# Optimization experiments

Measured on AMD Instinct MI355X. Metric: run time of the kernel, lower is better.

## Reference

```python
import jax, jax.numpy as jnp
import numpy as np

V, E, D = 50000, 800000, 128
EH, NH = 128, 128  # edge_hidden, node_hidden


def setup_inputs() -> dict:
    key = jax.random.key(0)
    ks = jax.random.split(key, 12)
    h = jax.random.normal(ks[0], (V, D), dtype=jnp.float32)
    edge_index = jax.random.randint(ks[1], (2, E), 0, V, dtype=jnp.int64)
    s = 0.02
    # edge MLP: Linear(2D->EH), Linear(EH->EH), Linear(EH->NH)
    W1 = jax.random.normal(ks[2], (2 * D, EH), dtype=jnp.float32) * s
    b1 = jnp.zeros((EH,), dtype=jnp.float32)
    W2 = jax.random.normal(ks[3], (EH, EH), dtype=jnp.float32) * s
    b2 = jnp.zeros((EH,), dtype=jnp.float32)
    W3 = jax.random.normal(ks[4], (EH, NH), dtype=jnp.float32) * s
    b3 = jnp.zeros((NH,), dtype=jnp.float32)
    # node MLP: Linear(D+NH->NH), Linear(NH->NH)
    Wn1 = jax.random.normal(ks[5], (D + NH, NH), dtype=jnp.float32) * s
    bn1 = jnp.zeros((NH,), dtype=jnp.float32)
    Wn2 = jax.random.normal(ks[6], (NH, NH), dtype=jnp.float32) * s
    bn2 = jnp.zeros((NH,), dtype=jnp.float32)
    return {"h": h, "edge_index": edge_index, "W1": W1, "b1": b1, "W2": W2,
            "b2": b2, "W3": W3, "b3": b3, "Wn1": Wn1, "bn1": bn1,
            "Wn2": Wn2, "bn2": bn2}


def reference(h, edge_index, W1, b1, W2, b2, W3, b3, Wn1, bn1, Wn2, bn2):
    src, dst = edge_index[0], edge_index[1]
    # gather node pairs -> edge features (E, 2D)
    edge_feat = jnp.concatenate([h[src], h[dst]], axis=-1)
    # 3-layer edge MLP
    m = jax.nn.relu(edge_feat @ W1 + b1)
    m = jax.nn.relu(m @ W2 + b2)
    messages = m @ W3 + b3                       # (E, NH)
    # scatter-add into destination nodes
    agg = jax.ops.segment_sum(messages, dst, num_segments=h.shape[0])  # (V, NH)
    # node MLP on [h, agg]
    x = jnp.concatenate([h, agg], axis=-1)       # (V, D+NH)
    out = jax.nn.relu(x @ Wn1 + bn1) @ Wn2 + bn2  # (V, NH)
    return out
```

## Files before the change

kernel.cpp:

```cpp
#include <hip/hip_runtime.h>

#define NV 50000
#define NE 800000
#define CVT_N 1600000
#define TR_N  81920
#define W3N_N 16384
#define B3N_N 128
#define NB1 49

typedef _Float16 f16x8 __attribute__((ext_vector_type(8)));
typedef _Float16 f16x4 __attribute__((ext_vector_type(4)));
typedef float    f32x4 __attribute__((ext_vector_type(4)));

static __device__ __forceinline__ f32x4 mfma16(f16x8 a, f16x8 b, f32x4 c) {
  return __builtin_amdgcn_mfma_f32_16x16x32_f16(a, b, c, 0, 0, 0);
}

__global__ void prep_kernel(const float* __restrict__ h, _Float16* __restrict__ hf,
    const float* __restrict__ W1, const float* __restrict__ W2, const float* __restrict__ W3,
    const float* __restrict__ Wn1, const float* __restrict__ Wn2, const float* __restrict__ b3,
    _Float16* __restrict__ w1st, _Float16* __restrict__ w1dt, _Float16* __restrict__ w2t,
    _Float16* __restrict__ wn1c, _Float16* __restrict__ wn2t, float* __restrict__ b3n,
    const int* __restrict__ ei, int* __restrict__ counts)
{
  int i = blockIdx.x * blockDim.x + threadIdx.x;
  if (i < CVT_N) {
    f32x4 v = reinterpret_cast<const f32x4*>(h)[i];
    f16x4 o;
    o[0] = (_Float16)v[0]; o[1] = (_Float16)v[1]; o[2] = (_Float16)v[2]; o[3] = (_Float16)v[3];
    reinterpret_cast<f16x4*>(hf)[i] = o;
    return;
  }
  i -= CVT_N;
  if (i < TR_N) {
    int seg = i >> 14;
    int j = i & 16383;
    int f = j >> 7, k = j & 127;
    switch (seg) {
      case 0: w1st[j] = (_Float16)W1[k * 128 + f]; break;
      case 1: w1dt[j] = (_Float16)W1[(k + 128) * 128 + f]; break;
      case 2: w2t[j]  = (_Float16)W2[k * 128 + f]; break;
      case 3: wn1c[f * 256 + k] = (_Float16)Wn1[k * 128 + f]; break;
      case 4: wn2t[j] = (_Float16)Wn2[k * 128 + f]; break;
    }
    return;
  }
  i -= TR_N;
  if (i < W3N_N) {
    int f = i >> 7, ii = i & 127;
    float a = 0.f;
    for (int j = 0; j < 128; j++) a += W3[ii * 128 + j] * Wn1[(128 + j) * 128 + f];
    wn1c[f * 256 + 128 + ii] = (_Float16)a;
    return;
  }
  i -= W3N_N;
  if (i < B3N_N) {
    float a = 0.f;
    for (int j = 0; j < 128; j++) a += b3[j] * Wn1[(128 + j) * 128 + i];
    b3n[i] = a;
    return;
  }
  i -= B3N_N;
  if (i < NE) atomicAdd(&counts[ei[NE + i]], 1);
}

__global__ __launch_bounds__(1024)
void bsum_kernel(const int* __restrict__ counts, int* __restrict__ bsum) {
  __shared__ int red[1024];
  const int t = threadIdx.x;
  int i = blockIdx.x * 1024 + t;
  red[t] = (i < NV) ? counts[i] : 0;
  __syncthreads();
  for (int off = 512; off > 0; off >>= 1) {
    if (t < off) red[t] += red[t + off];
    __syncthreads();
  }
  if (t == 0) bsum[blockIdx.x] = red[0];
}

__global__ void bscan_kernel(const int* __restrict__ bsum, int* __restrict__ boff) {
  if (threadIdx.x == 0 && blockIdx.x == 0) {
    int run = 0;
    for (int b = 0; b < NB1; b++) { boff[b] = run; run += bsum[b]; }
    boff[NB1] = run;
  }
}

__global__ __launch_bounds__(1024)
void offs_kernel(const int* __restrict__ counts, const int* __restrict__ boff,
                 int* __restrict__ offsets, int* __restrict__ cursor) {
  __shared__ int s[1024];
  const int t = threadIdx.x;
  int i = blockIdx.x * 1024 + t;
  int v = (i < NV) ? counts[i] : 0;
  s[t] = v;
  __syncthreads();
  for (int off = 1; off < 1024; off <<= 1) {
    int x = (t >= off) ? s[t - off] : 0;
    __syncthreads();
    s[t] += x;
    __syncthreads();
  }
  if (i < NV) {
    int excl = boff[blockIdx.x] + s[t] - v;
    offsets[i] = excl;
    cursor[i] = excl;
    if (i == NV - 1) offsets[NV] = boff[blockIdx.x] + s[t];
  }
}

__global__ void permute_kernel(const int* __restrict__ ei, int* __restrict__ cursor,
                               int2* __restrict__ pairs) {
  int e = blockIdx.x * blockDim.x + threadIdx.x;
  if (e < NE) {
    int s = ei[e], d = ei[NE + e];
    int pos = atomicAdd(&cursor[d], 1);
    pairs[pos] = make_int2(s, d);
  }
}

static __device__ __forceinline__ void gemm128_rows(
    const _Float16* __restrict__ hf, const int* nid, const _Float16* __restrict__ At,
    const float* __restrict__ bias, _Float16* __restrict__ Out,
    int nbase, int l15, int quad)
{
  f32x4 acc[8][4];
#pragma unroll
  for (int mt = 0; mt < 8; mt++)
#pragma unroll
    for (int nt = 0; nt < 4; nt++)
      acc[mt][nt] = (f32x4){0.f, 0.f, 0.f, 0.f};

  f16x8 Bc[4], Bn[4];
#pragma unroll
  for (int nt = 0; nt < 4; nt++)
    Bc[nt] = *reinterpret_cast<const f16x8*>(hf + (long long)nid[nt] * 128 + quad * 8);
#pragma unroll
  for (int s = 0; s < 4; s++) {
    if (s < 3) {
#pragma unroll
      for (int nt = 0; nt < 4; nt++)
        Bn[nt] = *reinterpret_cast<const f16x8*>(hf + (long long)nid[nt] * 128 + (s + 1) * 32 + quad * 8);
    }
    const int k = s * 32 + quad * 8;
#pragma unroll
    for (int mt = 0; mt < 8; mt++) {
      f16x8 A = *reinterpret_cast<const f16x8*>(At + (mt * 16 + l15) * 128 + k);
#pragma unroll
      for (int nt = 0; nt < 4; nt++)
        acc[mt][nt] = mfma16(A, Bc[nt], acc[mt][nt]);
    }
#pragma unroll
    for (int nt = 0; nt < 4; nt++) Bc[nt] = Bn[nt];
  }
#pragma unroll
  for (int mt = 0; mt < 8; mt++) {
    f32x4 bb = bias ? *reinterpret_cast<const f32x4*>(bias + mt * 16 + quad * 4)
                    : (f32x4){0.f, 0.f, 0.f, 0.f};
#pragma unroll
    for (int nt = 0; nt < 4; nt++) {
      int n = nbase + nt * 16 + l15;
      if (n < NV) {
        f16x4 o;
#pragma unroll
        for (int r = 0; r < 4; r++) o[r] = (_Float16)(acc[mt][nt][r] + bb[r]);
        *reinterpret_cast<f16x4*>(Out + (long long)n * 128 + mt * 16 + quad * 4) = o;
      }
    }
  }
}

__global__ __launch_bounds__(256, 2)
void h1_kernel(const _Float16* __restrict__ hf, const float* __restrict__ b1,
               const _Float16* __restrict__ w1st, const _Float16* __restrict__ w1dt,
               _Float16* __restrict__ H1s, _Float16* __restrict__ H1d)
{
  const int t = threadIdx.x;
  const int lane = t & 63, wave = t >> 6;
  const int quad = lane >> 4, l15 = lane & 15;
  const int nbase = blockIdx.x * 256 + wave * 64;
  int nid[4];
#pragma unroll
  for (int nt = 0; nt < 4; nt++) {
    int n = nbase + nt * 16 + l15;
    nid[nt] = n < NV ? n : NV - 1;
  }
  if (blockIdx.y == 0) gemm128_rows(hf, nid, w1st, nullptr, H1s, nbase, l15, quad);
  else                 gemm128_rows(hf, nid, w1dt, b1,      H1d, nbase, l15, quad);
}

__global__ __launch_bounds__(128, 2)
void edge_kernel(const _Float16* __restrict__ H1s, const _Float16* __restrict__ H1d,
                 const int2* __restrict__ pairs,
                 const _Float16* __restrict__ w2t, const float* __restrict__ b2,
                 float* __restrict__ agg2)
{
  __shared__ __align__(16) _Float16 M2t[128 * 128];
  __shared__ int sdst[128];
  __shared__ int segdst[128];
  __shared__ __align__(8) unsigned char sseg8[128];
  __shared__ unsigned long long wmask[2];
  __shared__ int snbr[2];

  const int t = threadIdx.x;
  const int lane = t & 63, wave = t >> 6;
  const int quad = lane >> 4, l15 = lane & 15;
  const int ebase = blockIdx.x * 128;
  const int wbase = wave * 64;

  { int2 pr = pairs[ebase + t]; sdst[t] = pr.y; }
  if (t == 0) snbr[0] = (ebase > 0) ? pairs[ebase - 1].y : -1;
  if (t == 1) snbr[1] = (ebase + 128 < NE) ? pairs[ebase + 128].y : -1;

  int esrc[4], edst[4];
#pragma unroll
  for (int et = 0; et < 4; et++) {
    int2 pr = pairs[ebase + wbase + et * 16 + l15];
    esrc[et] = pr.x; edst[et] = pr.y;
  }

  f16x8 m1f[4][4];
#pragma unroll
  for (int et = 0; et < 4; et++) {
#pragma unroll
    for (int s = 0; s < 4; s++) {
      f16x8 a = *reinterpret_cast<const f16x8*>(H1s + (long long)esrc[et] * 128 + s * 32 + quad * 8);
      f16x8 b = *reinterpret_cast<const f16x8*>(H1d + (long long)edst[et] * 128 + s * 32 + quad * 8);
      f16x8 o = a + b;
#pragma unroll
      for (int j = 0; j < 8; j++) o[j] = o[j] > (_Float16)0 ? o[j] : (_Float16)0;
      m1f[et][s] = o;
    }
  }

  __syncthreads();
  {
    bool flag = (t > 0) && (sdst[t] != sdst[t - 1]);
    unsigned long long bm = __ballot(flag);
    if (lane == 0) wmask[wave] = bm;
    int pre = __popcll(bm & ((1ull << lane) - 1ull)) + (flag ? 1 : 0);
    __syncthreads();
    int sid = pre + (wave ? (int)__popcll(wmask[0]) : 0);
    sseg8[t] = (unsigned char)sid;
    if (flag || t == 0) segdst[sid] = sdst[t];
  }

  float b2v[8];
#pragma unroll
  for (int ft = 0; ft < 8; ft++) b2v[ft] = b2[ft * 16 + l15];

  f32x4 acc[4][8];
#pragma unroll
  for (int et = 0; et < 4; et++)
#pragma unroll
    for (int ft = 0; ft < 8; ft++)
      acc[et][ft] = (f32x4){0.f, 0.f, 0.f, 0.f};

#pragma unroll
  for (int s = 0; s < 4; s++) {
    const int k = s * 32 + quad * 8;
#pragma unroll
    for (int ft = 0; ft < 8; ft++) {
      f16x8 B = *reinterpret_cast<const f16x8*>(w2t + (ft * 16 + l15) * 128 + k);
#pragma unroll
      for (int et = 0; et < 4; et++)
        acc[et][ft] = mfma16(m1f[et][s], B, acc[et][ft]);
    }
  }
#pragma unroll
  for (int et = 0; et < 4; et++) {
    const int g = wave * 16 + et * 4 + quad;
#pragma unroll
    for (int ft = 0; ft < 8; ft++) {
      const int f = ft * 16 + l15;
      f16x4 o;
#pragma unroll
      for (int r = 0; r < 4; r++) {
        float x = acc[et][ft][r] + b2v[ft];
        o[r] = (_Float16)(x > 0.f ? x : 0.f);
      }
      *reinterpret_cast<f16x4*>(&M2t[f * 128 + ((g ^ (l15 << 1)) * 4)]) = o;
    }
  }
  __syncthreads();

  const int nseg = (int)__popcll(wmask[0]) + (int)__popcll(wmask[1]) + 1;
  const int nmt = (nseg + 15) >> 4;
  const bool openL = (sdst[0] == snbr[0]);
  const bool openR = (sdst[127] == snbr[1]);

  f16x8 Bf[4][4];
#pragma unroll
  for (int fl = 0; fl < 4; fl++) {
    const int f = (wave * 4 + fl) * 16 + l15;
#pragma unroll
    for (int s = 0; s < 4; s++) {
      const int g0 = s * 8 + quad * 2;
      Bf[fl][s] = *reinterpret_cast<const f16x8*>(&M2t[f * 128 + ((g0 ^ (l15 << 1)) * 4)]);
    }
  }
  unsigned long long segb[4];
#pragma unroll
  for (int s = 0; s < 4; s++)
    segb[s] = *reinterpret_cast<const unsigned long long*>(&sseg8[s * 32 + quad * 8]);

  for (int mt = 0; mt < nmt; mt++) {
    const int myseg = mt * 16 + l15;
    f32x4 racc[4];
#pragma unroll
    for (int fl = 0; fl < 4; fl++) racc[fl] = (f32x4){0.f, 0.f, 0.f, 0.f};
#pragma unroll
    for (int s = 0; s < 4; s++) {
      f16x8 S;
#pragma unroll
      for (int j = 0; j < 8; j++)
        S[j] = ((int)((segb[s] >> (8 * j)) & 255ull) == myseg) ? (_Float16)1 : (_Float16)0;
#pragma unroll
      for (int fl = 0; fl < 4; fl++)
        racc[fl] = mfma16(S, Bf[fl][s], racc[fl]);
    }
#pragma unroll
    for (int fl = 0; fl < 4; fl++) {
      const int f = (wave * 4 + fl) * 16 + l15;
#pragma unroll
      for (int r = 0; r < 4; r++) {
        const int sg = mt * 16 + quad * 4 + r;
        if (sg < nseg) {
          float v = racc[fl][r];
          float* p = agg2 + (long long)segdst[sg] * 128 + f;
          const bool at = (sg == 0 && openL) || (sg == nseg - 1 && openR);
          if (at) unsafeAtomicAdd(p, v); else *p = v;
        }
      }
    }
  }
}

__global__ __launch_bounds__(256, 2)
void node_kernel(const _Float16* __restrict__ hf, const float* __restrict__ agg2,
                 const int* __restrict__ offsets,
                 const _Float16* __restrict__ wn1c, const float* __restrict__ bn1,
                 const float* __restrict__ b3n,
                 const _Float16* __restrict__ wn2t, const float* __restrict__ bn2,
                 float* __restrict__ out)
{
  __shared__ __align__(16) _Float16 M[256 * 128];
  const int t = threadIdx.x;
  const int lane = t & 63, wave = t >> 6;
  const int quad = lane >> 4, l15 = lane & 15;
  const int wbase = wave * 64;
  const int nbase = blockIdx.x * 256 + wbase;

  int nid[4]; float fcnt[4];
#pragma unroll
  for (int nt = 0; nt < 4; nt++) {
    int n = nbase + nt * 16 + l15;
    nid[nt] = n < NV ? n : NV - 1;
    fcnt[nt] = (n < NV) ? (float)(offsets[n + 1] - offsets[n]) : 0.f;
  }

  f32x4 acc[8][4];
#pragma unroll
  for (int mt = 0; mt < 8; mt++)
#pragma unroll
    for (int nt = 0; nt < 4; nt++)
      acc[mt][nt] = (f32x4){0.f, 0.f, 0.f, 0.f};

  f16x8 Bc[4], Bn[4];
#pragma unroll
  for (int nt = 0; nt < 4; nt++)
    Bc[nt] = *reinterpret_cast<const f16x8*>(hf + (long long)nid[nt] * 128 + quad * 8);
#pragma unroll
  for (int s = 0; s < 8; s++) {
    if (s < 7) {
      const int sn = s + 1;
      if (sn < 4) {
#pragma unroll
        for (int nt = 0; nt < 4; nt++)
          Bn[nt] = *reinterpret_cast<const f16x8*>(hf + (long long)nid[nt] * 128 + sn * 32 + quad * 8);
      } else {
#pragma unroll
        for (int nt = 0; nt < 4; nt++) {
          const float* ap = agg2 + (long long)nid[nt] * 128 + (sn - 4) * 32 + quad * 8;
          f32x4 a0 = *reinterpret_cast<const f32x4*>(ap);
          f32x4 a1 = *reinterpret_cast<const f32x4*>(ap + 4);
          f16x8 bb;
#pragma unroll
          for (int j = 0; j < 4; j++) { bb[j] = (_Float16)a0[j]; bb[4 + j] = (_Float16)a1[j]; }
          Bn[nt] = bb;
        }
      }
    }
    const int k = s * 32 + quad * 8;
#pragma unroll
    for (int mt = 0; mt < 8; mt++) {
      f16x8 A = *reinterpret_cast<const f16x8*>(wn1c + (mt * 16 + l15) * 256 + k);
#pragma unroll
      for (int nt = 0; nt < 4; nt++)
        acc[mt][nt] = mfma16(A, Bc[nt], acc[mt][nt]);
    }
#pragma unroll
    for (int nt = 0; nt < 4; nt++) Bc[nt] = Bn[nt];
  }
#pragma unroll
  for (int mt = 0; mt < 8; mt++) {
    f32x4 bb  = *reinterpret_cast<const f32x4*>(bn1 + mt * 16 + quad * 4);
    f32x4 b3c = *reinterpret_cast<const f32x4*>(b3n + mt * 16 + quad * 4);
    const int cbase = 2 * mt + (quad >> 1);
#pragma unroll
    for (int nt = 0; nt < 4; nt++) {
      int row = wbase + nt * 16 + l15;
      int c = cbase ^ (row & 15);
      f16x4 o;
#pragma unroll
      for (int r = 0; r < 4; r++) {
        float x = acc[mt][nt][r] + bb[r] + fcnt[nt] * b3c[r];
        o[r] = (_Float16)(x > 0.f ? x : 0.f);
      }
      *reinterpret_cast<f16x4*>(&M[row * 128 + c * 8 + (quad & 1) * 4]) = o;
      acc[mt][nt] = (f32x4){0.f, 0.f, 0.f, 0.f};
    }
  }

#pragma unroll
  for (int s = 0; s < 4; s++) {
    f16x8 B[4];
#pragma unroll
    for (int nt = 0; nt < 4; nt++) {
      int row = wbase + nt * 16 + l15;
      B[nt] = *reinterpret_cast<const f16x8*>(&M[row * 128 + (((4 * s + quad) ^ (row & 15)) * 8)]);
    }
    const int k = s * 32 + quad * 8;
#pragma unroll
    for (int mt = 0; mt < 8; mt++) {
      f16x8 A = *reinterpret_cast<const f16x8*>(wn2t + (mt * 16 + l15) * 128 + k);
#pragma unroll
      for (int nt = 0; nt < 4; nt++)
        acc[mt][nt] = mfma16(A, B[nt], acc[mt][nt]);
    }
  }
#pragma unroll
  for (int mt = 0; mt < 8; mt++) {
    f32x4 bias = *reinterpret_cast<const f32x4*>(bn2 + mt * 16 + quad * 4);
#pragma unroll
    for (int nt = 0; nt < 4; nt++) {
      int n = nbase + nt * 16 + l15;
      if (n < NV) {
        f32x4 v;
#pragma unroll
        for (int r = 0; r < 4; r++) v[r] = acc[mt][nt][r] + bias[r];
        *reinterpret_cast<f32x4*>(out + (long long)n * 128 + mt * 16 + quad * 4) = v;
      }
    }
  }
}

static inline size_t align16(size_t x) { return (x + 15) & ~(size_t)15; }

extern "C" void kernel_launch(void* const* d_in, const int* in_sizes, int n_in,
                              void* d_out, int out_size, void* d_ws, size_t ws_size,
                              hipStream_t stream)
{
  const float* h   = (const float*)d_in[0];
  const int*   ei  = (const int*)d_in[1];
  const float* W1  = (const float*)d_in[2];
  const float* b1  = (const float*)d_in[3];
  const float* W2  = (const float*)d_in[4];
  const float* b2  = (const float*)d_in[5];
  const float* W3  = (const float*)d_in[6];
  const float* b3  = (const float*)d_in[7];
  const float* Wn1 = (const float*)d_in[8];
  const float* bn1 = (const float*)d_in[9];
  const float* Wn2 = (const float*)d_in[10];
  const float* bn2 = (const float*)d_in[11];
  float* out = (float*)d_out;

  char* p = (char*)d_ws;
  _Float16* hf   = (_Float16*)p; p += align16((size_t)NV * 128 * 2);
  _Float16* H1s  = (_Float16*)p; p += align16((size_t)NV * 128 * 2);
  _Float16* H1d  = (_Float16*)p; p += align16((size_t)NV * 128 * 2);
  _Float16* w1st = (_Float16*)p; p += align16(128 * 128 * 2);
  _Float16* w1dt = (_Float16*)p; p += align16(128 * 128 * 2);
  _Float16* w2t  = (_Float16*)p; p += align16(128 * 128 * 2);
  _Float16* wn1c = (_Float16*)p; p += align16(128 * 256 * 2);
  _Float16* wn2t = (_Float16*)p; p += align16(128 * 128 * 2);
  float*  b3n  = (float*)p;  p += align16(128 * 4);
  int* counts  = (int*)p; p += align16((size_t)NV * 4);
  int* offsets = (int*)p; p += align16((size_t)(NV + 1) * 4);
  int* cursor  = (int*)p; p += align16((size_t)NV * 4);
  int* bsum    = (int*)p; p += align16((size_t)(NB1 + 1) * 4);
  int* boff    = (int*)p; p += align16((size_t)(NB1 + 1) * 4);
  int2* pairs  = (int2*)p; p += align16((size_t)NE * 8);
  float* agg2  = (float*)p; p += align16((size_t)NV * 128 * 4);

  hipMemsetAsync(counts, 0, (size_t)NV * 4, stream);
  hipMemsetAsync(agg2, 0, (size_t)NV * 128 * 4, stream);
  {
    int total = CVT_N + TR_N + W3N_N + B3N_N + NE;
    prep_kernel<<<(total + 255) / 256, 256, 0, stream>>>(
        h, hf, W1, W2, W3, Wn1, Wn2, b3,
        w1st, w1dt, w2t, wn1c, wn2t, b3n, ei, counts);
  }
  bsum_kernel<<<NB1, 1024, 0, stream>>>(counts, bsum);
  bscan_kernel<<<1, 64, 0, stream>>>(bsum, boff);
  offs_kernel<<<NB1, 1024, 0, stream>>>(counts, boff, offsets, cursor);
  permute_kernel<<<(NE + 255) / 256, 256, 0, stream>>>(ei, cursor, pairs);
  h1_kernel<<<dim3((NV + 255) / 256, 2), 256, 0, stream>>>(hf, b1, w1st, w1dt, H1s, H1d);
  edge_kernel<<<NE / 128, 128, 0, stream>>>(H1s, H1d, pairs, w2t, b2, agg2);
  node_kernel<<<(NV + 255) / 256, 256, 0, stream>>>(hf, agg2, offsets, wn1c, bn1, b3n,
                                                    wn2t, bn2, out);
}
```

Before: 349.1 us.

## Split edge layer-2 GEMM into two feature halves to halve LDS and raise occupancy

The edge kernel now computes the second MLP layer and the segment reduction in two passes of 64 output features each. This halves the shared M2t buffer, shrinks the accumulator register arrays, and raises launch bounds from 2 to 3 blocks per SIMD. Segment-boundary detection now reads the previous edge's destination straight from global memory instead of through a shared sdst array, which removes one barrier. The cost is an extra barrier per half, repeated segment-mask setup, and twice as many passes over the segment loop.

```diff
diff --git a/kernel.cpp b/kernel.cpp
--- a/kernel.cpp
+++ b/kernel.cpp
@@ -189,18 +189,17 @@
   else                 gemm128_rows(hf, nid, w1dt, b1,      H1d, nbase, l15, quad);
 }
 
-__global__ __launch_bounds__(128, 2)
+__global__ __launch_bounds__(128, 3)
 void edge_kernel(const _Float16* __restrict__ H1s, const _Float16* __restrict__ H1d,
                  const int2* __restrict__ pairs,
                  const _Float16* __restrict__ w2t, const float* __restrict__ b2,
                  float* __restrict__ agg2)
 {
-  __shared__ __align__(16) _Float16 M2t[128 * 128];
-  __shared__ int sdst[128];
+  __shared__ __align__(16) _Float16 M2t[64 * 128];
   __shared__ int segdst[128];
   __shared__ __align__(8) unsigned char sseg8[128];
   __shared__ unsigned long long wmask[2];
-  __shared__ int snbr[2];
+  __shared__ int sopen[2];
 
   const int t = threadIdx.x;
   const int lane = t & 63, wave = t >> 6;
@@ -208,9 +207,10 @@
   const int ebase = blockIdx.x * 128;
   const int wbase = wave * 64;
 
-  { int2 pr = pairs[ebase + t]; sdst[t] = pr.y; }
-  if (t == 0) snbr[0] = (ebase > 0) ? pairs[ebase - 1].y : -1;
-  if (t == 1) snbr[1] = (ebase + 128 < NE) ? pairs[ebase + 128].y : -1;
+  const int2 prt = pairs[ebase + t];
+  if (t == 0)   sopen[0] = (ebase > 0) && (prt.y == pairs[ebase - 1].y);
+  if (t == 127) sopen[1] = (ebase + 128 < NE) && (prt.y == pairs[ebase + 128].y);
+  const int dprev = (t > 0) ? pairs[ebase + t - 1].y : -1;
 
   int esrc[4], edst[4];
 #pragma unroll
@@ -233,103 +233,98 @@
     }
   }
 
+  const bool flag = (t > 0) && (prt.y != dprev);
+  unsigned long long bm = __ballot(flag);
+  if (lane == 0) wmask[wave] = bm;
+  int pre = __popcll(bm & ((1ull << lane) - 1ull)) + (flag ? 1 : 0);
   __syncthreads();
-  {
-    bool flag = (t > 0) && (sdst[t] != sdst[t - 1]);
-    unsigned long long bm = __ballot(flag);
-    if (lane == 0) wmask[wave] = bm;
-    int pre = __popcll(bm & ((1ull << lane) - 1ull)) + (flag ? 1 : 0);
-    __syncthreads();
-    int sid = pre + (wave ? (int)__popcll(wmask[0]) : 0);
-    sseg8[t] = (unsigned char)sid;
-    if (flag || t == 0) segdst[sid] = sdst[t];
-  }
-
-  float b2v[8];
-#pragma unroll
-  for (int ft = 0; ft < 8; ft++) b2v[ft] = b2[ft * 16 + l15];
-
-  f32x4 acc[4][8];
-#pragma unroll
-  for (int et = 0; et < 4; et++)
-#pragma unroll
-    for (int ft = 0; ft < 8; ft++)
-      acc[et][ft] = (f32x4){0.f, 0.f, 0.f, 0.f};
-
-#pragma unroll
-  for (int s = 0; s < 4; s++) {
-    const int k = s * 32 + quad * 8;
-#pragma unroll
-    for (int ft = 0; ft < 8; ft++) {
-      f16x8 B = *reinterpret_cast<const f16x8*>(w2t + (ft * 16 + l15) * 128 + k);
-#pragma unroll
-      for (int et = 0; et < 4; et++)
-        acc[et][ft] = mfma16(m1f[et][s], B, acc[et][ft]);
-    }
-  }
-#pragma unroll
-  for (int et = 0; et < 4; et++) {
-    const int g = wave * 16 + et * 4 + quad;
-#pragma unroll
-    for (int ft = 0; ft < 8; ft++) {
-      const int f = ft * 16 + l15;
-      f16x4 o;
-#pragma unroll
-      for (int r = 0; r < 4; r++) {
-        float x = acc[et][ft][r] + b2v[ft];
-        o[r] = (_Float16)(x > 0.f ? x : 0.f);
-      }
-      *reinterpret_cast<f16x4*>(&M2t[f * 128 + ((g ^ (l15 << 1)) * 4)]) = o;
-    }
-  }
-  __syncthreads();
-
+  const int sid = pre + (wave ? (int)__popcll(wmask[0]) : 0);
+  sseg8[t] = (unsigned char)sid;
+  if (flag || t == 0) segdst[sid] = prt.y;
   const int nseg = (int)__popcll(wmask[0]) + (int)__popcll(wmask[1]) + 1;
   const int nmt = (nseg + 15) >> 4;
-  const bool openL = (sdst[0] == snbr[0]);
-  const bool openR = (sdst[127] == snbr[1]);
-
-  f16x8 Bf[4][4];
-#pragma unroll
-  for (int fl = 0; fl < 4; fl++) {
-    const int f = (wave * 4 + fl) * 16 + l15;
+  const bool openL = sopen[0] != 0;
+  const bool openR = sopen[1] != 0;
+
+  for (int half = 0; half < 2; half++) {
+    f32x4 acc[4][4];
+#pragma unroll
+    for (int et = 0; et < 4; et++)
+#pragma unroll
+      for (int ft = 0; ft < 4; ft++)
+        acc[et][ft] = (f32x4){0.f, 0.f, 0.f, 0.f};
+
 #pragma unroll
     for (int s = 0; s < 4; s++) {
-      const int g0 = s * 8 + quad * 2;
-      Bf[fl][s] = *reinterpret_cast<const f16x8*>(&M2t[f * 128 + ((g0 ^ (l15 << 1)) * 4)]);
-    }
-  }
-  unsigned long long segb[4];
-#pragma unroll
-  for (int s = 0; s < 4; s++)
-    segb[s] = *reinterpret_cast<const unsigned long long*>(&sseg8[s * 32 + quad * 8]);
-
-  for (int mt = 0; mt < nmt; mt++) {
-    const int myseg = mt * 16 + l15;
-    f32x4 racc[4];
-#pragma unroll
-    for (int fl = 0; fl < 4; fl++) racc[fl] = (f32x4){0.f, 0.f, 0.f, 0.f};
-#pragma unroll
-    for (int s = 0; s < 4; s++) {
-      f16x8 S;
-#pragma unroll
-      for (int j = 0; j < 8; j++)
-        S[j] = ((int)((segb[s] >> (8 * j)) & 255ull) == myseg) ? (_Float16)1 : (_Float16)0;
-#pragma unroll
-      for (int fl = 0; fl < 4; fl++)
-        racc[fl] = mfma16(S, Bf[fl][s], racc[fl]);
-    }
-#pragma unroll
-    for (int fl = 0; fl < 4; fl++) {
-      const int f = (wave * 4 + fl) * 16 + l15;
-#pragma unroll
-      for (int r = 0; r < 4; r++) {
-        const int sg = mt * 16 + quad * 4 + r;
-        if (sg < nseg) {
-          float v = racc[fl][r];
-          float* p = agg2 + (long long)segdst[sg] * 128 + f;
-          const bool at = (sg == 0 && openL) || (sg == nseg - 1 && openR);
-          if (at) unsafeAtomicAdd(p, v); else *p = v;
+      const int k = s * 32 + quad * 8;
+#pragma unroll
+      for (int ft = 0; ft < 4; ft++) {
+        f16x8 B = *reinterpret_cast<const f16x8*>(w2t + ((half * 4 + ft) * 16 + l15) * 128 + k);
+#pragma unroll
+        for (int et = 0; et < 4; et++)
+          acc[et][ft] = mfma16(m1f[et][s], B, acc[et][ft]);
+      }
+    }
+#pragma unroll
+    for (int ft = 0; ft < 4; ft++) {
+      const float bv = b2[(half * 4 + ft) * 16 + l15];
+#pragma unroll
+      for (int et = 0; et < 4; et++) {
+        const int g = wave * 16 + et * 4 + quad;
+        f16x4 o;
+#pragma unroll
+        for (int r = 0; r < 4; r++) {
+          float x = acc[et][ft][r] + bv;
+          o[r] = (_Float16)(x > 0.f ? x : 0.f);
+        }
+        *reinterpret_cast<f16x4*>(&M2t[(ft * 16 + l15) * 128 + ((g ^ (l15 << 1)) * 4)]) = o;
+      }
+    }
+    __syncthreads();
+
+    f16x8 Bf[2][4];
+#pragma unroll
+    for (int fl = 0; fl < 2; fl++) {
+      const int flr = (wave * 2 + fl) * 16 + l15;
+#pragma unroll
+      for (int s = 0; s < 4; s++) {
+        const int g0 = s * 8 + quad * 2;
+        Bf[fl][s] = *reinterpret_cast<const f16x8*>(&M2t[flr * 128 + ((g0 ^ (l15 << 1)) * 4)]);
+      }
+    }
+    unsigned long long segb[4];
+#pragma unroll
+    for (int s = 0; s < 4; s++)
+      segb[s] = *reinterpret_cast<const unsigned long long*>(&sseg8[s * 32 + quad * 8]);
+    __syncthreads();
+
+    for (int mt = 0; mt < nmt; mt++) {
+      const int myseg = mt * 16 + l15;
+      f32x4 racc[2];
+#pragma unroll
+      for (int fl = 0; fl < 2; fl++) racc[fl] = (f32x4){0.f, 0.f, 0.f, 0.f};
+#pragma unroll
+      for (int s = 0; s < 4; s++) {
+        f16x8 S;
+#pragma unroll
+        for (int j = 0; j < 8; j++)
+          S[j] = ((int)((segb[s] >> (8 * j)) & 255ull) == myseg) ? (_Float16)1 : (_Float16)0;
+#pragma unroll
+        for (int fl = 0; fl < 2; fl++)
+          racc[fl] = mfma16(S, Bf[fl][s], racc[fl]);
+      }
+#pragma unroll
+      for (int fl = 0; fl < 2; fl++) {
+        const int f = half * 64 + (wave * 2 + fl) * 16 + l15;
+#pragma unroll
+        for (int r = 0; r < 4; r++) {
+          const int sg = mt * 16 + quad * 4 + r;
+          if (sg < nseg) {
+            float v = racc[fl][r];
+            float* p = agg2 + (long long)segdst[sg] * 128 + f;
+            const bool at = (sg == 0 && openL) || (sg == nseg - 1 && openR);
+            if (at) unsafeAtomicAdd(p, v); else *p = v;
+          }
         }
       }
     }
```

Result: slower. 385.7 us (+10.5%).
